# Kernel tuning notes

Hardware: AMD Instinct MI355X
Metric: run time of the kernel (lower is better)

The kernel has to match this reference:

```python
import jax, jax.numpy as jnp
import numpy as np

M_NODES = 49152  # HEALPix nside=64


def setup_inputs() -> dict:
    key = jax.random.key(0)
    ks = jax.random.split(key, 7)
    N, M, Fin, Fout, K, dm = 16, M_NODES, 32, 64, 5, 1
    E = 8 * M
    x = jax.random.normal(ks[0], (N, M, Fin), dtype=jnp.float32)
    # sparse Laplacian in COO form; small values keep Chebyshev recursion stable
    edge_vals = jax.random.normal(ks[1], (E,), dtype=jnp.float32) * 0.2
    edge_rows = jax.random.randint(ks[2], (E,), 0, M, dtype=jnp.int32)
    edge_cols = jax.random.randint(ks[3], (E,), 0, M, dtype=jnp.int32)
    dkernel = jax.random.normal(ks[4], (Fin, dm, K), dtype=jnp.float32) * (2.0 / K) ** 0.5
    pkernel = jax.random.normal(ks[5], (Fout, Fin * dm), dtype=jnp.float32) * (2.0 / (Fin * dm)) ** 0.5
    bias = jax.random.normal(ks[6], (1, 1, Fout), dtype=jnp.float32) * 0.01
    return {"x": x, "edge_vals": edge_vals, "dkernel": dkernel,
            "pkernel": pkernel, "bias": bias,
            "edge_rows": edge_rows, "edge_cols": edge_cols}


def reference(x, edge_vals, dkernel, pkernel, bias, edge_rows, edge_cols):
    N, M, Fin = x.shape
    _, dm, K = dkernel.shape
    Fout = pkernel.shape[0]

    def spmm(v):  # L @ v with L in COO, v: [M, C]
        return jax.ops.segment_sum(edge_vals[:, None] * v[edge_cols], edge_rows,
                                   num_segments=M)

    # x0: [M, N*Fin]
    x0 = jnp.transpose(x, (1, 0, 2)).reshape(M, N * Fin)
    stack = [x0]
    if K > 1:
        x1 = spmm(x0)
        stack.append(x1)
    for k in range(2, K):  # Chebyshev recursion T_k = 2 L T_{k-1} - T_{k-2}
        x2 = 2.0 * spmm(x1) - x0
        stack.append(x2)
        x0, x1 = x1, x2
    xs = jnp.stack(stack, axis=0)                      # [K, M, N*Fin]
    xs = xs.reshape(K, M, N, Fin)
    xs = jnp.transpose(xs, (3, 0, 2, 1)).reshape(Fin, K, N * M)
    y = jnp.einsum('fdk,fkp->fdp', dkernel, xs)        # depthwise: [Fin, dm, N*M]
    y = y.reshape(Fin * dm, N * M)
    y = pkernel @ y                                    # pointwise: [Fout, N*M]
    y = y.T.reshape(N, M, Fout)
    y = y + bias
    return jax.nn.relu(y)
```

## Files before the change

### kernel.cpp

```cpp
#include <hip/hip_runtime.h>


#define M_NODES 49152
#define FIN 32
#define KCH 5
#define FOUT 64
#define NB 16

typedef unsigned int u32;
typedef unsigned short u16;
typedef short bf16x8 __attribute__((ext_vector_type(8)));
typedef float f32x4 __attribute__((ext_vector_type(4)));

__device__ __forceinline__ float bflo(u32 w) { union { float f; u32 i; } v; v.i = w << 16; return v.f; }
__device__ __forceinline__ float bfhi(u32 w) { union { float f; u32 i; } v; v.i = w & 0xffff0000u; return v.f; }
__device__ __forceinline__ u32 f2bf(float f) {
    union { float f; u32 i; } v; v.f = f;
    u32 r = v.i + 0x7fffu + ((v.i >> 16) & 1u);
    return r >> 16;
}
__device__ __forceinline__ u32 pack2(float a, float b) { return f2bf(a) | (f2bf(b) << 16); }

__global__ void count_kernel(const int* __restrict__ rows, int* __restrict__ cnt, int E) {
    int e = blockIdx.x * 256 + threadIdx.x;
    if (e < E) atomicAdd(&cnt[rows[e]], 1);
}

__global__ void scan_kernel(int* __restrict__ cf, int* __restrict__ row_ptr, int M) {
    int tid = threadIdx.x;
    int lane = tid & 63;
    int wid = tid >> 6;
    __shared__ int wsum[16];
    __shared__ int chunk_total;
    int carry = 0;
    for (int base = 0; base < M; base += 1024) {
        int i = base + tid;
        int v = (i < M) ? cf[i] : 0;
        int x = v;
        #pragma unroll
        for (int off = 1; off < 64; off <<= 1) {
            int y = __shfl_up(x, off, 64);
            if (lane >= off) x += y;
        }
        if (lane == 63) wsum[wid] = x;
        __syncthreads();
        if (tid < 16) {
            int w = wsum[tid];
            int xx = w;
            #pragma unroll
            for (int off = 1; off < 16; off <<= 1) {
                int y = __shfl_up(xx, off, 64);
                if (tid >= off) xx += y;
            }
            wsum[tid] = xx - w;
            if (tid == 15) chunk_total = xx;
        }
        __syncthreads();
        int pos = carry + (x - v) + wsum[wid];
        if (i < M) { row_ptr[i] = pos; cf[i] = pos; }
        carry += chunk_total;
        __syncthreads();
    }
    if (tid == 0) row_ptr[M] = carry;
}

__global__ void scatter_kernel(const int* __restrict__ rows, const int* __restrict__ cols,
                               const float* __restrict__ vals, int* __restrict__ fill,
                               int2* __restrict__ edges, int E) {
    int e = blockIdx.x * 256 + threadIdx.x;
    if (e < E) {
        int r = rows[e];
        int pos = atomicAdd(&fill[r], 1);
        int2 ed; ed.x = cols[e]; ed.y = __float_as_int(vals[e]);
        edges[pos] = ed;
    }
}

__global__ __launch_bounds__(256) void cast_transpose_kernel(
    const float* __restrict__ x, uint4* __restrict__ T0, int M) {
    int m = blockIdx.x * 4 + (threadIdx.x >> 6);
    int l = threadIdx.x & 63;
    int n = l >> 2;
    int f0 = (l & 3) * 8;
    const float4* xp = (const float4*)(x + ((size_t)n * M + m) * FIN + f0);
    float4 a = xp[0], b = xp[1];
    uint4 o;
    o.x = pack2(a.x, a.y); o.y = pack2(a.z, a.w);
    o.z = pack2(b.x, b.y); o.w = pack2(b.z, b.w);
    T0[(size_t)m * 64 + l] = o;
}

__global__ void wprep_kernel(const float* __restrict__ dk, const float* __restrict__ pk,
                             u16* __restrict__ W) {
    int t = blockIdx.x * 256 + threadIdx.x;
    if (t < FOUT * KCH * FIN) {
        int fo = t / (KCH * FIN);
        int kf = t % (KCH * FIN);
        int kc = kf / FIN;
        int f  = kf % FIN;
        W[fo * (KCH * FIN) + kf] = (u16)f2bf(pk[fo * FIN + f] * dk[f * KCH + kc]);
    }
}

__device__ __forceinline__ void acc8(float* r, uint4 g, float v) {
    r[0] = fmaf(v, bflo(g.x), r[0]); r[1] = fmaf(v, bfhi(g.x), r[1]);
    r[2] = fmaf(v, bflo(g.y), r[2]); r[3] = fmaf(v, bfhi(g.y), r[3]);
    r[4] = fmaf(v, bflo(g.z), r[4]); r[5] = fmaf(v, bfhi(g.z), r[5]);
    r[6] = fmaf(v, bflo(g.w), r[6]); r[7] = fmaf(v, bfhi(g.w), r[7]);
}

template<int FIRST>
__global__ __launch_bounds__(256) void spmm_kernel(
    const uint4* __restrict__ Tin, const uint4* __restrict__ Tprev, uint4* __restrict__ Tout,
    const int* __restrict__ row_ptr, const int2* __restrict__ edges, int M) {
    int m = blockIdx.x * 4 + (threadIdx.x >> 6);
    int l = threadIdx.x & 63;
    int e = row_ptr[m];
    int e_end = row_ptr[m + 1];
    float r[8] = {0.f, 0.f, 0.f, 0.f, 0.f, 0.f, 0.f, 0.f};
    for (; e + 4 <= e_end; e += 4) {
        int2 e0 = edges[e], e1 = edges[e + 1], e2 = edges[e + 2], e3 = edges[e + 3];
        uint4 g0 = Tin[(size_t)e0.x * 64 + l];
        uint4 g1 = Tin[(size_t)e1.x * 64 + l];
        uint4 g2 = Tin[(size_t)e2.x * 64 + l];
        uint4 g3 = Tin[(size_t)e3.x * 64 + l];
        acc8(r, g0, __int_as_float(e0.y));
        acc8(r, g1, __int_as_float(e1.y));
        acc8(r, g2, __int_as_float(e2.y));
        acc8(r, g3, __int_as_float(e3.y));
    }
    for (; e < e_end; ++e) {
        int2 ed = edges[e];
        uint4 g = Tin[(size_t)ed.x * 64 + l];
        acc8(r, g, __int_as_float(ed.y));
    }
    if (!FIRST) {
        uint4 p = Tprev[(size_t)m * 64 + l];
        r[0] = fmaf(2.f, r[0], -bflo(p.x)); r[1] = fmaf(2.f, r[1], -bfhi(p.x));
        r[2] = fmaf(2.f, r[2], -bflo(p.y)); r[3] = fmaf(2.f, r[3], -bfhi(p.y));
        r[4] = fmaf(2.f, r[4], -bflo(p.z)); r[5] = fmaf(2.f, r[5], -bfhi(p.z));
        r[6] = fmaf(2.f, r[6], -bflo(p.w)); r[7] = fmaf(2.f, r[7], -bfhi(p.w));
    }
    uint4 o;
    o.x = pack2(r[0], r[1]); o.y = pack2(r[2], r[3]);
    o.z = pack2(r[4], r[5]); o.w = pack2(r[6], r[7]);
    Tout[(size_t)m * 64 + l] = o;
}

__global__ __launch_bounds__(256) void pw_mfma_kernel(
    const uint4* __restrict__ T, const uint4* __restrict__ W4,
    const float* __restrict__ bias, float* __restrict__ out, int M) {
    __shared__ uint4 lds[2][1024];
    int t = threadIdx.x;
    int w = t >> 6;
    int l = t & 63;
    int lr = l & 15;
    int lg = l >> 4;
    int m0 = blockIdx.x * 16;
    const size_t kstride = (size_t)M * 64;
    const uint4* tile_base = T + (size_t)m0 * 64;

    float bv[4];
    #pragma unroll
    for (int fo = 0; fo < 4; ++fo) bv[fo] = bias[fo * 16 + lr];

    f32x4 acc[4][4];
    #pragma unroll
    for (int nn = 0; nn < 4; ++nn)
        #pragma unroll
        for (int fo = 0; fo < 4; ++fo)
            acc[nn][fo] = (f32x4){bv[fo], bv[fo], bv[fo], bv[fo]};

    uint4 sreg[4];
    #pragma unroll
    for (int j = 0; j < 4; ++j) sreg[j] = tile_base[(size_t)j * 256 + t];
    #pragma unroll
    for (int j = 0; j < 4; ++j) {
        int idx = j * 256 + t;
        int row = idx >> 6, c = idx & 63;
        lds[0][row * 64 + (c ^ (row & 7))] = sreg[j];
    }
    __syncthreads();

    for (int kc = 0; kc < KCH; ++kc) {
        uint4 nreg[4];
        if (kc < KCH - 1) {
            const uint4* src = tile_base + (size_t)(kc + 1) * kstride;
            #pragma unroll
            for (int j = 0; j < 4; ++j) nreg[j] = src[(size_t)j * 256 + t];
        }
        bf16x8 bfr[4];
        #pragma unroll
        for (int fo = 0; fo < 4; ++fo) {
            uint4 wv = W4[(fo * 16 + lr) * 20 + kc * 4 + lg];
            bfr[fo] = *(bf16x8*)&wv;
        }
        const uint4* buf = lds[kc & 1];
        #pragma unroll
        for (int nn = 0; nn < 4; ++nn) {
            int n_g = w * 4 + nn;
            uint4 a = buf[lr * 64 + ((n_g * 4 + lg) ^ (lr & 7))];
            bf16x8 af = *(bf16x8*)&a;
            #pragma unroll
            for (int fo = 0; fo < 4; ++fo)
                acc[nn][fo] = __builtin_amdgcn_mfma_f32_16x16x32_bf16(af, bfr[fo], acc[nn][fo], 0, 0, 0);
        }
        if (kc < KCH - 1) {
            uint4* buf2 = lds[(kc + 1) & 1];
            #pragma unroll
            for (int j = 0; j < 4; ++j) {
                int idx = j * 256 + t;
                int row = idx >> 6, c = idx & 63;
                buf2[row * 64 + (c ^ (row & 7))] = nreg[j];
            }
        }
        __syncthreads();
    }

    #pragma unroll
    for (int nn = 0; nn < 4; ++nn) {
        int n_g = w * 4 + nn;
        #pragma unroll
        for (int fo = 0; fo < 4; ++fo) {
            float* op = out + ((size_t)n_g * M + m0 + lg * 4) * FOUT + fo * 16 + lr;
            #pragma unroll
            for (int rr = 0; rr < 4; ++rr)
                __builtin_nontemporal_store(fmaxf(acc[nn][fo][rr], 0.f), op + (size_t)rr * FOUT);
        }
    }
}

extern "C" void kernel_launch(void* const* d_in, const int* in_sizes, int n_in,
                              void* d_out, int out_size, void* d_ws, size_t ws_size,
                              hipStream_t stream) {
    const float* x         = (const float*)d_in[0];
    const float* edge_vals = (const float*)d_in[1];
    const float* dk        = (const float*)d_in[2];
    const float* pk        = (const float*)d_in[3];
    const float* bias      = (const float*)d_in[4];
    const int*   erow      = (const int*)d_in[5];
    const int*   ecol      = (const int*)d_in[6];
    float* out = (float*)d_out;

    const int M = M_NODES;
    const int E = in_sizes[1];

    size_t t_words = (size_t)M * 64;
    uint4* T       = (uint4*)d_ws;
    u16*   W       = (u16*)(T + 5 * t_words);
    int*   row_ptr = (int*)(W + FOUT * KCH * FIN);
    int*   fill    = row_ptr + (M + 1);
    int2*  edges   = (int2*)(fill + M);

    uint4* T0 = T;
    uint4* T1 = T + 1 * t_words;
    uint4* T2 = T + 2 * t_words;
    uint4* T3 = T + 3 * t_words;
    uint4* T4 = T + 4 * t_words;

    hipMemsetAsync(fill, 0, (size_t)M * sizeof(int), stream);
    count_kernel<<<(E + 255) / 256, 256, 0, stream>>>(erow, fill, E);
    scan_kernel<<<1, 1024, 0, stream>>>(fill, row_ptr, M);
    scatter_kernel<<<(E + 255) / 256, 256, 0, stream>>>(erow, ecol, edge_vals, fill, edges, E);

    cast_transpose_kernel<<<M / 4, 256, 0, stream>>>(x, T0, M);
    wprep_kernel<<<(FOUT * KCH * FIN + 255) / 256, 256, 0, stream>>>(dk, pk, W);

    spmm_kernel<1><<<M / 4, 256, 0, stream>>>(T0, T0, T1, row_ptr, edges, M);
    spmm_kernel<0><<<M / 4, 256, 0, stream>>>(T1, T0, T2, row_ptr, edges, M);
    spmm_kernel<0><<<M / 4, 256, 0, stream>>>(T2, T1, T3, row_ptr, edges, M);
    spmm_kernel<0><<<M / 4, 256, 0, stream>>>(T3, T2, T4, row_ptr, edges, M);

    pw_mfma_kernel<<<M / 16, 256, 0, stream>>>(T, (const uint4*)W, bias, out, M);
}
```

Before: 480.6 us.

## Parallelize CSR scan per-thread chunks and deepen SpMM gather unrolling

The single-block scan now has each of 1024 threads own a contiguous 48-element chunk. Each thread loads its chunk with int4 vectors, does one block-wide scan of the chunk sums, and writes prefix offsets back vectorized, replacing the 48 serial block iterations, each with three barriers. The SpMM kernel unrolls the edge gather to 8 in flight and hoists the Tprev load ahead of the loop to raise memory-level parallelism. The fill pointer is padded so the int4 accesses stay 16-byte aligned. This costs more registers per thread in both kernels.

```diff
diff --git a/kernel.cpp b/kernel.cpp
--- a/kernel.cpp
+++ b/kernel.cpp
@@ -26,42 +26,56 @@
     if (e < E) atomicAdd(&cnt[rows[e]], 1);
 }
 
-__global__ void scan_kernel(int* __restrict__ cf, int* __restrict__ row_ptr, int M) {
+__global__ __launch_bounds__(1024) void scan_kernel(int* __restrict__ cf,
+                                                    int* __restrict__ row_ptr, int M) {
+    const int CH = M_NODES / 1024;
     int tid = threadIdx.x;
     int lane = tid & 63;
     int wid = tid >> 6;
+    int base = tid * CH;
+
+    int4 v[CH / 4];
+    const int4* src = (const int4*)(cf + base);
+    int sum = 0;
+    #pragma unroll
+    for (int j = 0; j < CH / 4; ++j) {
+        v[j] = src[j];
+        sum += v[j].x + v[j].y + v[j].z + v[j].w;
+    }
+    int x = sum;
+    #pragma unroll
+    for (int off = 1; off < 64; off <<= 1) {
+        int y = __shfl_up(x, off, 64);
+        if (lane >= off) x += y;
+    }
     __shared__ int wsum[16];
-    __shared__ int chunk_total;
-    int carry = 0;
-    for (int base = 0; base < M; base += 1024) {
-        int i = base + tid;
-        int v = (i < M) ? cf[i] : 0;
-        int x = v;
-        #pragma unroll
-        for (int off = 1; off < 64; off <<= 1) {
-            int y = __shfl_up(x, off, 64);
-            if (lane >= off) x += y;
-        }
-        if (lane == 63) wsum[wid] = x;
-        __syncthreads();
-        if (tid < 16) {
-            int w = wsum[tid];
-            int xx = w;
-            #pragma unroll
-            for (int off = 1; off < 16; off <<= 1) {
-                int y = __shfl_up(xx, off, 64);
-                if (tid >= off) xx += y;
-            }
-            wsum[tid] = xx - w;
-            if (tid == 15) chunk_total = xx;
-        }
-        __syncthreads();
-        int pos = carry + (x - v) + wsum[wid];
-        if (i < M) { row_ptr[i] = pos; cf[i] = pos; }
-        carry += chunk_total;
-        __syncthreads();
-    }
-    if (tid == 0) row_ptr[M] = carry;
+    if (lane == 63) wsum[wid] = x;
+    __syncthreads();
+    if (tid < 16) {
+        int w = wsum[tid];
+        int xx = w;
+        #pragma unroll
+        for (int off = 1; off < 16; off <<= 1) {
+            int y = __shfl_up(xx, off, 64);
+            if (tid >= off) xx += y;
+        }
+        wsum[tid] = xx - w;
+    }
+    __syncthreads();
+    int run = (x - sum) + wsum[wid];
+    int4* rp = (int4*)(row_ptr + base);
+    int4* cc = (int4*)(cf + base);
+    #pragma unroll
+    for (int j = 0; j < CH / 4; ++j) {
+        int4 o;
+        o.x = run;           run += v[j].x;
+        o.y = run;           run += v[j].y;
+        o.z = run;           run += v[j].z;
+        o.w = run;           run += v[j].w;
+        rp[j] = o;
+        cc[j] = o;
+    }
+    if (tid == 1023) row_ptr[M] = run;
 }
 
 __global__ void scatter_kernel(const int* __restrict__ rows, const int* __restrict__ cols,
@@ -117,17 +131,29 @@
     int l = threadIdx.x & 63;
     int e = row_ptr[m];
     int e_end = row_ptr[m + 1];
+    uint4 p;
+    if (!FIRST) p = Tprev[(size_t)m * 64 + l];
     float r[8] = {0.f, 0.f, 0.f, 0.f, 0.f, 0.f, 0.f, 0.f};
-    for (; e + 4 <= e_end; e += 4) {
-        int2 e0 = edges[e], e1 = edges[e + 1], e2 = edges[e + 2], e3 = edges[e + 3];
-        uint4 g0 = Tin[(size_t)e0.x * 64 + l];
-        uint4 g1 = Tin[(size_t)e1.x * 64 + l];
-        uint4 g2 = Tin[(size_t)e2.x * 64 + l];
-        uint4 g3 = Tin[(size_t)e3.x * 64 + l];
-        acc8(r, g0, __int_as_float(e0.y));
-        acc8(r, g1, __int_as_float(e1.y));
-        acc8(r, g2, __int_as_float(e2.y));
-        acc8(r, g3, __int_as_float(e3.y));
+    for (; e + 8 <= e_end; e += 8) {
+        int2 ed[8];
+        #pragma unroll
+        for (int j = 0; j < 8; ++j) ed[j] = edges[e + j];
+        uint4 g[8];
+        #pragma unroll
+        for (int j = 0; j < 8; ++j) g[j] = Tin[(size_t)ed[j].x * 64 + l];
+        #pragma unroll
+        for (int j = 0; j < 8; ++j) acc8(r, g[j], __int_as_float(ed[j].y));
+    }
+    if (e + 4 <= e_end) {
+        int2 ed[4];
+        #pragma unroll
+        for (int j = 0; j < 4; ++j) ed[j] = edges[e + j];
+        uint4 g[4];
+        #pragma unroll
+        for (int j = 0; j < 4; ++j) g[j] = Tin[(size_t)ed[j].x * 64 + l];
+        #pragma unroll
+        for (int j = 0; j < 4; ++j) acc8(r, g[j], __int_as_float(ed[j].y));
+        e += 4;
     }
     for (; e < e_end; ++e) {
         int2 ed = edges[e];
@@ -135,7 +161,6 @@
         acc8(r, g, __int_as_float(ed.y));
     }
     if (!FIRST) {
-        uint4 p = Tprev[(size_t)m * 64 + l];
         r[0] = fmaf(2.f, r[0], -bflo(p.x)); r[1] = fmaf(2.f, r[1], -bfhi(p.x));
         r[2] = fmaf(2.f, r[2], -bflo(p.y)); r[3] = fmaf(2.f, r[3], -bfhi(p.y));
         r[4] = fmaf(2.f, r[4], -bflo(p.z)); r[5] = fmaf(2.f, r[5], -bfhi(p.z));
@@ -249,7 +274,7 @@
     uint4* T       = (uint4*)d_ws;
     u16*   W       = (u16*)(T + 5 * t_words);
     int*   row_ptr = (int*)(W + FOUT * KCH * FIN);
-    int*   fill    = row_ptr + (M + 1);
+    int*   fill    = row_ptr + (M + 4);
     int2*  edges   = (int2*)(fill + M);
 
     uint4* T0 = T;
```

New measurement: 440.9 us. -8.3%, faster.
